# Kernel tuning notes

Hardware: AMD Instinct MI355X
Metric: run time of the kernel (lower is better)

Reference implementation:

```python
import jax, jax.numpy as jnp
import numpy as np

N = 50000
E = 800000
EP = 200000
IN_C = 128
HID = 128


def setup_inputs() -> dict:
    key = jax.random.key(0)
    ks = jax.random.split(key, 10)
    x = jax.random.normal(ks[0], (N, IN_C), dtype=jnp.float32)
    edge_index = jax.random.randint(ks[1], (2, E), 0, N, dtype=jnp.int64)
    pred_edges = jax.random.randint(ks[2], (2, EP), 0, N, dtype=jnp.int64)
    s_in = 1.0 / np.sqrt(IN_C)
    s_h = 1.0 / np.sqrt(HID)
    W1l = jax.random.normal(ks[3], (IN_C, HID), dtype=jnp.float32) * s_in
    W1r = jax.random.normal(ks[4], (IN_C, HID), dtype=jnp.float32) * s_in
    b1 = jnp.zeros((HID,), dtype=jnp.float32)
    W2l = jax.random.normal(ks[5], (HID, HID), dtype=jnp.float32) * s_h
    W2r = jax.random.normal(ks[6], (HID, HID), dtype=jnp.float32) * s_h
    b2 = jnp.zeros((HID,), dtype=jnp.float32)
    return {"x": x, "W1l": W1l, "b1": b1, "W1r": W1r,
            "W2l": W2l, "b2": b2, "W2r": W2r,
            "edge_index": edge_index, "pred_edges": pred_edges}


def _sage_conv(h, Wl, b, Wr, src, dst, n_nodes):
    # PyG SAGEConv (aggr='mean'): out = lin_l(mean_j x_j) + lin_r(x_i)
    msg = h[src]                                              # (E, D) gather
    agg = jax.ops.segment_sum(msg, dst, num_segments=n_nodes)  # (N, D) scatter-add
    deg = jax.ops.segment_sum(jnp.ones((src.shape[0],), h.dtype), dst,
                              num_segments=n_nodes)
    agg = agg / jnp.maximum(deg, 1.0)[:, None]                # mean (0 for isolated)
    return agg @ Wl + b + h @ Wr


def reference(x, W1l, b1, W1r, W2l, b2, W2r, edge_index, pred_edges):
    n_nodes = x.shape[0]
    src, dst = edge_index[0], edge_index[1]
    h = jax.nn.relu(_sage_conv(x, W1l, b1, W1r, src, dst, n_nodes))
    z = _sage_conv(h, W2l, b2, W2r, src, dst, n_nodes)
    ps, pd = pred_edges[0], pred_edges[1]
    return jnp.sum(z[ps] * z[pd], axis=-1)  # (E_pred,) logits
```

## Files before the change

### kernel.cpp

```cpp
#include <hip/hip_runtime.h>

#define D 128

typedef __attribute__((ext_vector_type(8))) short short8;
typedef __attribute__((ext_vector_type(4))) float f32x4;

__device__ inline unsigned int f2bf_bits(float f) {
    unsigned int u = __float_as_uint(f);
    return (u + 0x7FFFu + ((u >> 16) & 1u)) >> 16;
}

__global__ __launch_bounds__(256) void cast_bf16_kernel(const float* __restrict__ in,
                                                        unsigned short* __restrict__ outb,
                                                        int n4,
                                                        int* __restrict__ chist,
                                                        int* __restrict__ csrpad) {
    if (blockIdx.x == gridDim.x - 1) {
        int t = threadIdx.x;
        chist[t] = 0;
        if (t < 16) csrpad[t] = 0;
        return;
    }
    int i = blockIdx.x * blockDim.x + threadIdx.x;
    if (i >= n4) return;
    f32x4 v = *(const f32x4*)(in + (size_t)i * 4);
    ushort4 o;
    o.x = (unsigned short)f2bf_bits(v.x);
    o.y = (unsigned short)f2bf_bits(v.y);
    o.z = (unsigned short)f2bf_bits(v.z);
    o.w = (unsigned short)f2bf_bits(v.w);
    *(ushort4*)(outb + (size_t)i * 4) = o;
}

__global__ __launch_bounds__(256) void coarse_count_kernel(const int* __restrict__ dst,
                                                           int* __restrict__ chist, int E) {
    __shared__ int h[256];
    h[threadIdx.x] = 0;
    __syncthreads();
    const int stride = gridDim.x * 256;
    for (int e = blockIdx.x * 256 + threadIdx.x; e < E; e += stride)
        atomicAdd(&h[dst[e] >> 8], 1);
    __syncthreads();
    int v = h[threadIdx.x];
    if (v) atomicAdd(&chist[threadIdx.x], v);
}

__global__ __launch_bounds__(256) void scan256_kernel(const int* __restrict__ chist,
                                                      int* __restrict__ cbase,
                                                      int* __restrict__ gcur) {
    __shared__ int wsum[4];
    const int t = threadIdx.x, lane = t & 63, wv = t >> 6;
    int v = chist[t];
    int s = v;
#pragma unroll
    for (int o = 1; o < 64; o <<= 1) {
        int u = __shfl_up(s, o, 64);
        if (lane >= o) s += u;
    }
    if (lane == 63) wsum[wv] = s;
    __syncthreads();
    int add = 0;
    for (int w = 0; w < wv; ++w) add += wsum[w];
    cbase[t + 1] = s + add;
    if (t == 0) cbase[0] = 0;
    gcur[t] = s + add - v;
}

#define CCHUNK 4096
__global__ __launch_bounds__(256) void coarse_scatter_kernel(
    const int* __restrict__ src, const int* __restrict__ dst,
    int* __restrict__ gcur, unsigned int* __restrict__ centries, int E)
{
    __shared__ int h[256];
    __shared__ int base[256];
    __shared__ unsigned int stage[CCHUNK];
    const int t = threadIdx.x;
    const int e0 = blockIdx.x * CCHUNK;
    h[t] = 0;
    __syncthreads();
#pragma unroll
    for (int i = 0; i < 16; ++i) {
        int e = e0 + i * 256 + t;
        unsigned int u = 0xFFFFFFFFu;
        if (e < E) {
            int d = dst[e];
            int s = src[e];
            int b = d >> 8;
            u = ((unsigned)b << 24) | ((unsigned)s << 8) | (unsigned)(d & 255);
            atomicAdd(&h[b], 1);
        }
        stage[i * 256 + t] = u;
    }
    __syncthreads();
    base[t] = atomicAdd(&gcur[t], h[t]);
    __syncthreads();
    h[t] = 0;
    __syncthreads();
#pragma unroll
    for (int i = 0; i < 16; ++i) {
        unsigned int u = stage[i * 256 + t];
        if (u != 0xFFFFFFFFu) {
            int b = u >> 24;
            int r = atomicAdd(&h[b], 1);
            centries[base[b] + r] = u & 0x00FFFFFFu;
        }
    }
}

#define DCAP 8192
__global__ __launch_bounds__(256) void fine_bucket_kernel(
    const unsigned int* __restrict__ centries,
    const int* __restrict__ cbase,
    int* __restrict__ offo, int* __restrict__ csr, int N, int E)
{
    __shared__ int h[256], ex[256], wsum[4];
    __shared__ int stg[DCAP];
    const int t = threadIdx.x, lane = t & 63, wv = t >> 6;
    const int b = blockIdx.x;
    const int s0 = cbase[b];
    const int cnt = cbase[b + 1] - s0;
    h[t] = 0;
    __syncthreads();
    for (int i = t; i < cnt; i += 256)
        atomicAdd(&h[centries[s0 + i] & 255], 1);
    __syncthreads();
    int v = h[t], s = v;
#pragma unroll
    for (int o = 1; o < 64; o <<= 1) {
        int u = __shfl_up(s, o, 64);
        if (lane >= o) s += u;
    }
    if (lane == 63) wsum[wv] = s;
    __syncthreads();
    int add = 0;
    for (int w = 0; w < wv; ++w) add += wsum[w];
    const int exc = s + add - v;
    ex[t] = exc;
    const int dg = b * 256 + t;
    if (dg < N) offo[dg] = s0 + exc;
    if (b == 0 && t == 0) offo[N] = E;
    h[t] = 0;
    __syncthreads();
    if (cnt <= DCAP) {
        for (int i = t; i < cnt; i += 256) {
            unsigned int u = centries[s0 + i];
            int dl = u & 255;
            int r = atomicAdd(&h[dl], 1);
            stg[ex[dl] + r] = (int)(u >> 8);
        }
        __syncthreads();
        for (int i = t; i < cnt; i += 256)
            csr[s0 + i] = stg[i];
    } else {
        for (int i = t; i < cnt; i += 256) {
            unsigned int u = centries[s0 + i];
            int dl = u & 255;
            int r = atomicAdd(&h[dl], 1);
            csr[s0 + ex[dl] + r] = (int)(u >> 8);
        }
    }
}

__global__ __launch_bounds__(256) void wsplit_kernel(const float* __restrict__ W1l,
                                                     const float* __restrict__ W1r,
                                                     const float* __restrict__ W2l,
                                                     const float* __restrict__ W2r,
                                                     unsigned short* __restrict__ h1,
                                                     unsigned short* __restrict__ l1,
                                                     unsigned short* __restrict__ h2,
                                                     unsigned short* __restrict__ l2) {
    int gidx = blockIdx.x * 256 + threadIdx.x;
    int sel = gidx >> 15;
    int idx = gidx & 32767;
    int t = idx >> 12;
    int ks = (idx >> 9) & 7;
    int lane = (idx >> 3) & 63;
    int j = idx & 7;
    int q = lane >> 4, r16 = lane & 15;
    int k = ks * 32 + q * 8 + j;
    int c = t * 16 + r16;
    const float* Wl = sel ? W2l : W1l;
    const float* Wr = sel ? W2r : W1r;
    float v = (k < 128) ? Wl[k * 128 + c] : Wr[(k - 128) * 128 + c];
    unsigned int h = f2bf_bits(v);
    float hf = __uint_as_float(h << 16);
    unsigned int l = f2bf_bits(v - hf);
    (sel ? h2 : h1)[idx] = (unsigned short)h;
    (sel ? l2 : l1)[idx] = (unsigned short)l;
}

__global__ __launch_bounds__(256) void gather_mean_kernel(
    const unsigned short* __restrict__ featbf,
    const int* __restrict__ off,
    const int* __restrict__ csr,
    float* __restrict__ aggp,
    int n_nodes)
{
    const int hw = (blockIdx.x * 256 + threadIdx.x) >> 5;
    const int l5 = threadIdx.x & 31;
    if (hw >= n_nodes) return;
    const unsigned short* fb = featbf + (size_t)l5 * 4;
    const int start = off[hw];
    const int end = off[hw + 1];
    f32x4 acc = {0.f, 0.f, 0.f, 0.f};
    for (int e = start; e < end; e += 16) {
        int4 ia = *(const int4*)(csr + e);
        int4 ib = *(const int4*)(csr + e + 4);
        int4 ic = *(const int4*)(csr + e + 8);
        int4 id = *(const int4*)(csr + e + 12);
        uint2 r[16];
        r[0]  = *(const uint2*)(fb + (size_t)ia.x * D);
        r[1]  = *(const uint2*)(fb + (size_t)ia.y * D);
        r[2]  = *(const uint2*)(fb + (size_t)ia.z * D);
        r[3]  = *(const uint2*)(fb + (size_t)ia.w * D);
        r[4]  = *(const uint2*)(fb + (size_t)ib.x * D);
        r[5]  = *(const uint2*)(fb + (size_t)ib.y * D);
        r[6]  = *(const uint2*)(fb + (size_t)ib.z * D);
        r[7]  = *(const uint2*)(fb + (size_t)ib.w * D);
        r[8]  = *(const uint2*)(fb + (size_t)ic.x * D);
        r[9]  = *(const uint2*)(fb + (size_t)ic.y * D);
        r[10] = *(const uint2*)(fb + (size_t)ic.z * D);
        r[11] = *(const uint2*)(fb + (size_t)ic.w * D);
        r[12] = *(const uint2*)(fb + (size_t)id.x * D);
        r[13] = *(const uint2*)(fb + (size_t)id.y * D);
        r[14] = *(const uint2*)(fb + (size_t)id.z * D);
        r[15] = *(const uint2*)(fb + (size_t)id.w * D);
#pragma unroll
        for (int p = 0; p < 16; ++p) {
            uint2 rv = r[p];
            if (e + p >= end) { rv.x = 0u; rv.y = 0u; }
            acc.x += __uint_as_float(rv.x << 16);
            acc.y += __uint_as_float(rv.x & 0xffff0000u);
            acc.z += __uint_as_float(rv.y << 16);
            acc.w += __uint_as_float(rv.y & 0xffff0000u);
        }
    }
    float dinv = 1.0f / (float)max(end - start, 1);
    acc *= dinv;
    const int tile = hw >> 4, r16 = hw & 15;
    const int ks = l5 >> 3, q = (l5 & 7) >> 1, jb = (l5 & 1) * 4;
    const size_t p = ((size_t)(tile * 4 + ks) * 64 + q * 16 + r16) * 8 + jb;
    *(f32x4*)(aggp + p) = acc;
}

__global__ __launch_bounds__(256) void sage_gemm_kernel(
    const float* __restrict__ aggp,
    const float* __restrict__ selfm,
    const unsigned short* __restrict__ wpk_hi,
    const unsigned short* __restrict__ wpk_lo,
    const float* __restrict__ bias,
    float* __restrict__ outp,
    unsigned short* __restrict__ outbf,
    int ntiles, int self_packed, int do_relu)
{
    const int wv = threadIdx.x >> 6;
    const int lane = threadIdx.x & 63;
    const int tile = blockIdx.x * 4 + wv;
    if (tile >= ntiles) return;
    const int q = lane >> 4, r16 = lane & 15;
    const int n0w = tile * 16;

    f32x4 acc8[8];
#pragma unroll
    for (int t = 0; t < 8; ++t) acc8[t] = (f32x4){0.f, 0.f, 0.f, 0.f};

    const float* ap = aggp + (size_t)tile * 2048 + lane * 8;
    const float* spk = selfm + (size_t)tile * 2048 + lane * 8;
    const float* spr = selfm + (size_t)(n0w + r16) * D + q * 8;

    for (int ks = 0; ks < 8; ++ks) {
        f32x4 a0, a1;
        if (ks < 4) {
            a0 = *(const f32x4*)(ap + ks * 512);
            a1 = *(const f32x4*)(ap + ks * 512 + 4);
        } else if (self_packed) {
            a0 = *(const f32x4*)(spk + (ks - 4) * 512);
            a1 = *(const f32x4*)(spk + (ks - 4) * 512 + 4);
        } else {
            a0 = *(const f32x4*)(spr + (ks - 4) * 32);
            a1 = *(const f32x4*)(spr + (ks - 4) * 32 + 4);
        }
        short8 BH[8], BL[8];
        const unsigned short* bh = wpk_hi + (size_t)ks * 512 + lane * 8;
        const unsigned short* bl = wpk_lo + (size_t)ks * 512 + lane * 8;
#pragma unroll
        for (int t = 0; t < 8; ++t) {
            BH[t] = *(const short8*)(bh + (size_t)t * 4096);
            BL[t] = *(const short8*)(bl + (size_t)t * 4096);
        }
        short8 ahi, alo;
#pragma unroll
        for (int i = 0; i < 8; ++i) {
            float vv = (i < 4) ? a0[i] : a1[i - 4];
            unsigned int h = f2bf_bits(vv);
            float hf = __uint_as_float(h << 16);
            unsigned int l = f2bf_bits(vv - hf);
            ahi[i] = (short)h;
            alo[i] = (short)l;
        }
#pragma unroll
        for (int t = 0; t < 8; ++t) {
            acc8[t] = __builtin_amdgcn_mfma_f32_16x16x32_bf16(ahi, BH[t], acc8[t], 0, 0, 0);
            acc8[t] = __builtin_amdgcn_mfma_f32_16x16x32_bf16(alo, BH[t], acc8[t], 0, 0, 0);
            acc8[t] = __builtin_amdgcn_mfma_f32_16x16x32_bf16(ahi, BL[t], acc8[t], 0, 0, 0);
        }
    }

#pragma unroll
    for (int t = 0; t < 8; ++t) {
        const float bv = bias[t * 16 + r16];
#pragma unroll
        for (int r = 0; r < 4; ++r) {
            float vv = acc8[t][r] + bv;
            if (do_relu) vv = fmaxf(vv, 0.f);
            if (outp) {
                const size_t p = ((size_t)(tile * 4 + (t >> 1)) * 64
                                  + ((t & 1) * 2 + (r16 >> 3)) * 16 + q * 4 + r) * 8
                                 + (r16 & 7);
                outp[p] = vv;
            }
            if (outbf) {
                outbf[(size_t)(n0w + q * 4 + r) * D + t * 16 + r16] =
                    (unsigned short)f2bf_bits(vv);
            }
        }
    }
}

__global__ __launch_bounds__(256) void pred_kernel(const unsigned short* __restrict__ zbf,
                                                   const int* __restrict__ ps,
                                                   const int* __restrict__ pd,
                                                   float* __restrict__ out, int EP) {
    int idx = blockIdx.x * blockDim.x + threadIdx.x;
    int e = idx >> 5;
    if (e >= EP) return;
    int l = idx & 31;
    const unsigned short* fb = zbf + (size_t)l * 4;
    uint2 ra = *(const uint2*)(fb + (size_t)ps[e] * D);
    uint2 rb = *(const uint2*)(fb + (size_t)pd[e] * D);
    float p = __uint_as_float(ra.x << 16)         * __uint_as_float(rb.x << 16)
            + __uint_as_float(ra.x & 0xffff0000u) * __uint_as_float(rb.x & 0xffff0000u)
            + __uint_as_float(ra.y << 16)         * __uint_as_float(rb.y << 16)
            + __uint_as_float(ra.y & 0xffff0000u) * __uint_as_float(rb.y & 0xffff0000u);
#pragma unroll
    for (int off = 16; off > 0; off >>= 1) p += __shfl_xor(p, off, 32);
    if (l == 0) out[e] = p;
}

extern "C" void kernel_launch(void* const* d_in, const int* in_sizes, int n_in,
                              void* d_out, int out_size, void* d_ws, size_t ws_size,
                              hipStream_t stream) {
    const float* x   = (const float*)d_in[0];
    const float* W1l = (const float*)d_in[1];
    const float* b1  = (const float*)d_in[2];
    const float* W1r = (const float*)d_in[3];
    const float* W2l = (const float*)d_in[4];
    const float* b2  = (const float*)d_in[5];
    const float* W2r = (const float*)d_in[6];
    const int* edge_index = (const int*)d_in[7];
    const int* pred_edges = (const int*)d_in[8];
    float* out = (float*)d_out;

    const int N  = in_sizes[0] / D;
    const int E  = in_sizes[7] / 2;
    const int EP = in_sizes[8] / 2;

    const int* src = edge_index;
    const int* dst = edge_index + E;
    const int* ps  = pred_edges;
    const int* pd  = pred_edges + EP;

    int* chist   = (int*)d_ws;
    int* cbase   = chist + 256;
    int* gcur    = cbase + 272;
    int* off     = gcur + 256;
    unsigned int* centries = (unsigned int*)(off + 50016);
    int* csr     = (int*)(centries + E);
    float* aggp  = (float*)(csr + E + 16);
    float* hpk   = aggp + (size_t)N * D;
    unsigned short* w1_hi = (unsigned short*)(hpk + (size_t)N * D);
    unsigned short* w1_lo = w1_hi + 32768;
    unsigned short* w2_hi = w1_lo + 32768;
    unsigned short* w2_lo = w2_hi + 32768;
    unsigned short* fbf   = w2_lo + 32768;

    const int nblk_gather = (N * 32 + 255) / 256;
    const int ntiles = N / 16;
    const int nblk_gemm = (ntiles + 3) / 4;
    const int ncast = (N * D / 4 + 255) / 256;
    const int nbC = (E + CCHUNK - 1) / CCHUNK;
    const int nbD = (N + 255) / 256;

    wsplit_kernel<<<256, 256, 0, stream>>>(W1l, W1r, W2l, W2r, w1_hi, w1_lo, w2_hi, w2_lo);
    cast_bf16_kernel<<<ncast + 1, 256, 0, stream>>>(x, fbf, N * D / 4, chist, csr + E);

    coarse_count_kernel<<<256, 256, 0, stream>>>(dst, chist, E);
    scan256_kernel<<<1, 256, 0, stream>>>(chist, cbase, gcur);
    coarse_scatter_kernel<<<nbC, 256, 0, stream>>>(src, dst, gcur, centries, E);
    fine_bucket_kernel<<<nbD, 256, 0, stream>>>(centries, cbase, off, csr, N, E);

    gather_mean_kernel<<<nblk_gather, 256, 0, stream>>>(fbf, off, csr, aggp, N);
    sage_gemm_kernel<<<nblk_gemm, 256, 0, stream>>>(aggp, x, w1_hi, w1_lo, b1,
                                                    hpk, fbf, ntiles, 0, 1);
    gather_mean_kernel<<<nblk_gather, 256, 0, stream>>>(fbf, off, csr, aggp, N);
    sage_gemm_kernel<<<nblk_gemm, 256, 0, stream>>>(aggp, hpk, w2_hi, w2_lo, b2,
                                                    (float*)nullptr, fbf, ntiles, 1, 0);
    pred_kernel<<<(EP * 32 + 255) / 256, 256, 0, stream>>>(fbf, ps, pd, out, EP);
}
```

Before: 257.3 us.

## Store activations as bf16 hi/lo pairs and widen gather loads to 16 bytes

```diff
diff --git a/kernel.cpp b/kernel.cpp
--- a/kernel.cpp
+++ b/kernel.cpp
@@ -10,26 +10,61 @@
     return (u + 0x7FFFu + ((u >> 16) & 1u)) >> 16;
 }
 
-__global__ __launch_bounds__(256) void cast_bf16_kernel(const float* __restrict__ in,
-                                                        unsigned short* __restrict__ outb,
-                                                        int n4,
-                                                        int* __restrict__ chist,
-                                                        int* __restrict__ csrpad) {
-    if (blockIdx.x == gridDim.x - 1) {
-        int t = threadIdx.x;
+__device__ inline float bfhi(unsigned int u) { return __uint_as_float(u << 16); }
+__device__ inline float bflo(unsigned int u) { return __uint_as_float(u & 0xffff0000u); }
+
+__global__ __launch_bounds__(256) void prep_kernel(
+    const float* __restrict__ x,
+    const float* __restrict__ W1l, const float* __restrict__ W1r,
+    const float* __restrict__ W2l, const float* __restrict__ W2r,
+    unsigned short* __restrict__ xbf, unsigned short* __restrict__ xlo,
+    unsigned short* __restrict__ h1, unsigned short* __restrict__ l1,
+    unsigned short* __restrict__ h2, unsigned short* __restrict__ l2,
+    int n4, int ncast, int* __restrict__ chist, int* __restrict__ csrpad)
+{
+    const int b = blockIdx.x;
+    const int t = threadIdx.x;
+    if (b < ncast) {
+        int i = b * 256 + t;
+        if (i >= n4) return;
+        f32x4 v = *(const f32x4*)(x + (size_t)i * 4);
+        ushort4 oh, ol;
+        {
+            unsigned int h; float hf;
+            h = f2bf_bits(v.x); hf = __uint_as_float(h << 16);
+            oh.x = (unsigned short)h; ol.x = (unsigned short)f2bf_bits(v.x - hf);
+            h = f2bf_bits(v.y); hf = __uint_as_float(h << 16);
+            oh.y = (unsigned short)h; ol.y = (unsigned short)f2bf_bits(v.y - hf);
+            h = f2bf_bits(v.z); hf = __uint_as_float(h << 16);
+            oh.z = (unsigned short)h; ol.z = (unsigned short)f2bf_bits(v.z - hf);
+            h = f2bf_bits(v.w); hf = __uint_as_float(h << 16);
+            oh.w = (unsigned short)h; ol.w = (unsigned short)f2bf_bits(v.w - hf);
+        }
+        *(ushort4*)(xbf + (size_t)i * 4) = oh;
+        *(ushort4*)(xlo + (size_t)i * 4) = ol;
+    } else if (b < ncast + 256) {
+        int gidx = (b - ncast) * 256 + t;
+        int sel = gidx >> 15;
+        int idx = gidx & 32767;
+        int tt = idx >> 12;
+        int ks = (idx >> 9) & 7;
+        int lane = (idx >> 3) & 63;
+        int j = idx & 7;
+        int qq = lane >> 4, r16 = lane & 15;
+        int k = ks * 32 + qq * 8 + j;
+        int c = tt * 16 + r16;
+        const float* Wl = sel ? W2l : W1l;
+        const float* Wr = sel ? W2r : W1r;
+        float v = (k < 128) ? Wl[k * 128 + c] : Wr[(k - 128) * 128 + c];
+        unsigned int h = f2bf_bits(v);
+        float hf = __uint_as_float(h << 16);
+        unsigned int l = f2bf_bits(v - hf);
+        (sel ? h2 : h1)[idx] = (unsigned short)h;
+        (sel ? l2 : l1)[idx] = (unsigned short)l;
+    } else {
         chist[t] = 0;
         if (t < 16) csrpad[t] = 0;
-        return;
-    }
-    int i = blockIdx.x * blockDim.x + threadIdx.x;
-    if (i >= n4) return;
-    f32x4 v = *(const f32x4*)(in + (size_t)i * 4);
-    ushort4 o;
-    o.x = (unsigned short)f2bf_bits(v.x);
-    o.y = (unsigned short)f2bf_bits(v.y);
-    o.z = (unsigned short)f2bf_bits(v.z);
-    o.w = (unsigned short)f2bf_bits(v.w);
-    *(ushort4*)(outb + (size_t)i * 4) = o;
+    }
 }
 
 __global__ __launch_bounds__(256) void coarse_count_kernel(const int* __restrict__ dst,
@@ -161,97 +196,81 @@
     }
 }
 
-__global__ __launch_bounds__(256) void wsplit_kernel(const float* __restrict__ W1l,
-                                                     const float* __restrict__ W1r,
-                                                     const float* __restrict__ W2l,
-                                                     const float* __restrict__ W2r,
-                                                     unsigned short* __restrict__ h1,
-                                                     unsigned short* __restrict__ l1,
-                                                     unsigned short* __restrict__ h2,
-                                                     unsigned short* __restrict__ l2) {
-    int gidx = blockIdx.x * 256 + threadIdx.x;
-    int sel = gidx >> 15;
-    int idx = gidx & 32767;
-    int t = idx >> 12;
-    int ks = (idx >> 9) & 7;
-    int lane = (idx >> 3) & 63;
-    int j = idx & 7;
-    int q = lane >> 4, r16 = lane & 15;
-    int k = ks * 32 + q * 8 + j;
-    int c = t * 16 + r16;
-    const float* Wl = sel ? W2l : W1l;
-    const float* Wr = sel ? W2r : W1r;
-    float v = (k < 128) ? Wl[k * 128 + c] : Wr[(k - 128) * 128 + c];
-    unsigned int h = f2bf_bits(v);
-    float hf = __uint_as_float(h << 16);
-    unsigned int l = f2bf_bits(v - hf);
-    (sel ? h2 : h1)[idx] = (unsigned short)h;
-    (sel ? l2 : l1)[idx] = (unsigned short)l;
-}
-
 __global__ __launch_bounds__(256) void gather_mean_kernel(
     const unsigned short* __restrict__ featbf,
     const int* __restrict__ off,
     const int* __restrict__ csr,
-    float* __restrict__ aggp,
+    unsigned short* __restrict__ agg_hi,
+    unsigned short* __restrict__ agg_lo,
     int n_nodes)
 {
-    const int hw = (blockIdx.x * 256 + threadIdx.x) >> 5;
-    const int l5 = threadIdx.x & 31;
+    const int hw = (blockIdx.x * 256 + threadIdx.x) >> 4;
+    const int L = threadIdx.x & 15;
     if (hw >= n_nodes) return;
-    const unsigned short* fb = featbf + (size_t)l5 * 4;
+    const unsigned short* fb = featbf + (size_t)L * 8;
     const int start = off[hw];
     const int end = off[hw + 1];
-    f32x4 acc = {0.f, 0.f, 0.f, 0.f};
+    float acc[8] = {0.f, 0.f, 0.f, 0.f, 0.f, 0.f, 0.f, 0.f};
     for (int e = start; e < end; e += 16) {
         int4 ia = *(const int4*)(csr + e);
         int4 ib = *(const int4*)(csr + e + 4);
         int4 ic = *(const int4*)(csr + e + 8);
         int4 id = *(const int4*)(csr + e + 12);
-        uint2 r[16];
-        r[0]  = *(const uint2*)(fb + (size_t)ia.x * D);
-        r[1]  = *(const uint2*)(fb + (size_t)ia.y * D);
-        r[2]  = *(const uint2*)(fb + (size_t)ia.z * D);
-        r[3]  = *(const uint2*)(fb + (size_t)ia.w * D);
-        r[4]  = *(const uint2*)(fb + (size_t)ib.x * D);
-        r[5]  = *(const uint2*)(fb + (size_t)ib.y * D);
-        r[6]  = *(const uint2*)(fb + (size_t)ib.z * D);
-        r[7]  = *(const uint2*)(fb + (size_t)ib.w * D);
-        r[8]  = *(const uint2*)(fb + (size_t)ic.x * D);
-        r[9]  = *(const uint2*)(fb + (size_t)ic.y * D);
-        r[10] = *(const uint2*)(fb + (size_t)ic.z * D);
-        r[11] = *(const uint2*)(fb + (size_t)ic.w * D);
-        r[12] = *(const uint2*)(fb + (size_t)id.x * D);
-        r[13] = *(const uint2*)(fb + (size_t)id.y * D);
-        r[14] = *(const uint2*)(fb + (size_t)id.z * D);
-        r[15] = *(const uint2*)(fb + (size_t)id.w * D);
+        uint4 r[16];
+        r[0]  = *(const uint4*)(fb + (size_t)ia.x * D);
+        r[1]  = *(const uint4*)(fb + (size_t)ia.y * D);
+        r[2]  = *(const uint4*)(fb + (size_t)ia.z * D);
+        r[3]  = *(const uint4*)(fb + (size_t)ia.w * D);
+        r[4]  = *(const uint4*)(fb + (size_t)ib.x * D);
+        r[5]  = *(const uint4*)(fb + (size_t)ib.y * D);
+        r[6]  = *(const uint4*)(fb + (size_t)ib.z * D);
+        r[7]  = *(const uint4*)(fb + (size_t)ib.w * D);
+        r[8]  = *(const uint4*)(fb + (size_t)ic.x * D);
+        r[9]  = *(const uint4*)(fb + (size_t)ic.y * D);
+        r[10] = *(const uint4*)(fb + (size_t)ic.z * D);
+        r[11] = *(const uint4*)(fb + (size_t)ic.w * D);
+        r[12] = *(const uint4*)(fb + (size_t)id.x * D);
+        r[13] = *(const uint4*)(fb + (size_t)id.y * D);
+        r[14] = *(const uint4*)(fb + (size_t)id.z * D);
+        r[15] = *(const uint4*)(fb + (size_t)id.w * D);
 #pragma unroll
         for (int p = 0; p < 16; ++p) {
-            uint2 rv = r[p];
-            if (e + p >= end) { rv.x = 0u; rv.y = 0u; }
-            acc.x += __uint_as_float(rv.x << 16);
-            acc.y += __uint_as_float(rv.x & 0xffff0000u);
-            acc.z += __uint_as_float(rv.y << 16);
-            acc.w += __uint_as_float(rv.y & 0xffff0000u);
-        }
-    }
-    float dinv = 1.0f / (float)max(end - start, 1);
-    acc *= dinv;
+            uint4 rv = r[p];
+            if (e + p >= end) { rv.x = 0u; rv.y = 0u; rv.z = 0u; rv.w = 0u; }
+            acc[0] += bfhi(rv.x); acc[1] += bflo(rv.x);
+            acc[2] += bfhi(rv.y); acc[3] += bflo(rv.y);
+            acc[4] += bfhi(rv.z); acc[5] += bflo(rv.z);
+            acc[6] += bfhi(rv.w); acc[7] += bflo(rv.w);
+        }
+    }
+    const float dinv = 1.0f / (float)max(end - start, 1);
+    short8 hi8, lo8;
+#pragma unroll
+    for (int i = 0; i < 8; ++i) {
+        float v = acc[i] * dinv;
+        unsigned int h = f2bf_bits(v);
+        float hf = __uint_as_float(h << 16);
+        hi8[i] = (short)h;
+        lo8[i] = (short)f2bf_bits(v - hf);
+    }
     const int tile = hw >> 4, r16 = hw & 15;
-    const int ks = l5 >> 3, q = (l5 & 7) >> 1, jb = (l5 & 1) * 4;
-    const size_t p = ((size_t)(tile * 4 + ks) * 64 + q * 16 + r16) * 8 + jb;
-    *(f32x4*)(aggp + p) = acc;
+    const int ks = L >> 2, qq = L & 3;
+    const size_t p = ((size_t)(tile * 4 + ks) * 64 + qq * 16 + r16) * 8;
+    *(short8*)(agg_hi + p) = hi8;
+    *(short8*)(agg_lo + p) = lo8;
 }
 
 __global__ __launch_bounds__(256) void sage_gemm_kernel(
-    const float* __restrict__ aggp,
-    const float* __restrict__ selfm,
+    const unsigned short* __restrict__ agg_hi,
+    const unsigned short* __restrict__ agg_lo,
+    const unsigned short* __restrict__ self_hi,
+    const unsigned short* __restrict__ self_lo,
     const unsigned short* __restrict__ wpk_hi,
     const unsigned short* __restrict__ wpk_lo,
     const float* __restrict__ bias,
-    float* __restrict__ outp,
-    unsigned short* __restrict__ outbf,
-    int ntiles, int self_packed, int do_relu)
+    unsigned short* __restrict__ out_hi,
+    unsigned short* __restrict__ out_lo,
+    int ntiles, int do_relu)
 {
     const int wv = threadIdx.x >> 6;
     const int lane = threadIdx.x & 63;
@@ -264,21 +283,19 @@
 #pragma unroll
     for (int t = 0; t < 8; ++t) acc8[t] = (f32x4){0.f, 0.f, 0.f, 0.f};
 
-    const float* ap = aggp + (size_t)tile * 2048 + lane * 8;
-    const float* spk = selfm + (size_t)tile * 2048 + lane * 8;
-    const float* spr = selfm + (size_t)(n0w + r16) * D + q * 8;
+    const unsigned short* aph = agg_hi + (size_t)tile * 2048 + lane * 8;
+    const unsigned short* apl = agg_lo + (size_t)tile * 2048 + lane * 8;
+    const unsigned short* sph = self_hi + (size_t)(n0w + r16) * D + q * 8;
+    const unsigned short* spl = self_lo + (size_t)(n0w + r16) * D + q * 8;
 
     for (int ks = 0; ks < 8; ++ks) {
-        f32x4 a0, a1;
+        short8 ahi, alo;
         if (ks < 4) {
-            a0 = *(const f32x4*)(ap + ks * 512);
-            a1 = *(const f32x4*)(ap + ks * 512 + 4);
-        } else if (self_packed) {
-            a0 = *(const f32x4*)(spk + (ks - 4) * 512);
-            a1 = *(const f32x4*)(spk + (ks - 4) * 512 + 4);
+            ahi = *(const short8*)(aph + ks * 512);
+            alo = *(const short8*)(apl + ks * 512);
         } else {
-            a0 = *(const f32x4*)(spr + (ks - 4) * 32);
-            a1 = *(const f32x4*)(spr + (ks - 4) * 32 + 4);
+            ahi = *(const short8*)(sph + (ks - 4) * 32);
+            alo = *(const short8*)(spl + (ks - 4) * 32);
         }
         short8 BH[8], BL[8];
         const unsigned short* bh = wpk_hi + (size_t)ks * 512 + lane * 8;
@@ -287,16 +304,6 @@
         for (int t = 0; t < 8; ++t) {
             BH[t] = *(const short8*)(bh + (size_t)t * 4096);
             BL[t] = *(const short8*)(bl + (size_t)t * 4096);
-        }
-        short8 ahi, alo;
-#pragma unroll
-        for (int i = 0; i < 8; ++i) {
-            float vv = (i < 4) ? a0[i] : a1[i - 4];
-            unsigned int h = f2bf_bits(vv);
-            float hf = __uint_as_float(h << 16);
-            unsigned int l = f2bf_bits(vv - hf);
-            ahi[i] = (short)h;
-            alo[i] = (short)l;
         }
 #pragma unroll
         for (int t = 0; t < 8; ++t) {
@@ -313,15 +320,12 @@
         for (int r = 0; r < 4; ++r) {
             float vv = acc8[t][r] + bv;
             if (do_relu) vv = fmaxf(vv, 0.f);
-            if (outp) {
-                const size_t p = ((size_t)(tile * 4 + (t >> 1)) * 64
-                                  + ((t & 1) * 2 + (r16 >> 3)) * 16 + q * 4 + r) * 8
-                                 + (r16 & 7);
-                outp[p] = vv;
-            }
-            if (outbf) {
-                outbf[(size_t)(n0w + q * 4 + r) * D + t * 16 + r16] =
-                    (unsigned short)f2bf_bits(vv);
+            const size_t o = (size_t)(n0w + q * 4 + r) * D + t * 16 + r16;
+            unsigned int h = f2bf_bits(vv);
+            out_hi[o] = (unsigned short)h;
+            if (out_lo) {
+                float hf = __uint_as_float(h << 16);
+                out_lo[o] = (unsigned short)f2bf_bits(vv - hf);
             }
         }
     }
@@ -331,20 +335,20 @@
                                                    const int* __restrict__ ps,
                                                    const int* __restrict__ pd,
                                                    float* __restrict__ out, int EP) {
-    int idx = blockIdx.x * blockDim.x + threadIdx.x;
-    int e = idx >> 5;
+    int idx = blockIdx.x * 256 + threadIdx.x;
+    int e = idx >> 4;
     if (e >= EP) return;
-    int l = idx & 31;
-    const unsigned short* fb = zbf + (size_t)l * 4;
-    uint2 ra = *(const uint2*)(fb + (size_t)ps[e] * D);
-    uint2 rb = *(const uint2*)(fb + (size_t)pd[e] * D);
-    float p = __uint_as_float(ra.x << 16)         * __uint_as_float(rb.x << 16)
-            + __uint_as_float(ra.x & 0xffff0000u) * __uint_as_float(rb.x & 0xffff0000u)
-            + __uint_as_float(ra.y << 16)         * __uint_as_float(rb.y << 16)
-            + __uint_as_float(ra.y & 0xffff0000u) * __uint_as_float(rb.y & 0xffff0000u);
-#pragma unroll
-    for (int off = 16; off > 0; off >>= 1) p += __shfl_xor(p, off, 32);
-    if (l == 0) out[e] = p;
+    int L = idx & 15;
+    const unsigned short* fb = zbf + (size_t)L * 8;
+    uint4 ra = *(const uint4*)(fb + (size_t)ps[e] * D);
+    uint4 rb = *(const uint4*)(fb + (size_t)pd[e] * D);
+    float p = bfhi(ra.x) * bfhi(rb.x) + bflo(ra.x) * bflo(rb.x)
+            + bfhi(ra.y) * bfhi(rb.y) + bflo(ra.y) * bflo(rb.y)
+            + bfhi(ra.z) * bfhi(rb.z) + bflo(ra.z) * bflo(rb.z)
+            + bfhi(ra.w) * bfhi(rb.w) + bflo(ra.w) * bflo(rb.w);
+#pragma unroll
+    for (int off = 8; off > 0; off >>= 1) p += __shfl_xor(p, off, 16);
+    if (L == 0) out[e] = p;
 }
 
 extern "C" void kernel_launch(void* const* d_in, const int* in_sizes, int n_in,
@@ -376,34 +380,42 @@
     int* off     = gcur + 256;
     unsigned int* centries = (unsigned int*)(off + 50016);
     int* csr     = (int*)(centries + E);
-    float* aggp  = (float*)(csr + E + 16);
-    float* hpk   = aggp + (size_t)N * D;
-    unsigned short* w1_hi = (unsigned short*)(hpk + (size_t)N * D);
+    unsigned short* w1_hi = (unsigned short*)(csr + E + 16);
     unsigned short* w1_lo = w1_hi + 32768;
     unsigned short* w2_hi = w1_lo + 32768;
     unsigned short* w2_lo = w2_hi + 32768;
-    unsigned short* fbf   = w2_lo + 32768;
-
-    const int nblk_gather = (N * 32 + 255) / 256;
+    unsigned short* xbf   = w2_lo + 32768;
+    unsigned short* xlo   = xbf + (size_t)N * D;
+    unsigned short* hbf   = xlo + (size_t)N * D;
+    unsigned short* hlo   = hbf + (size_t)N * D;
+    unsigned short* zbf   = hlo + (size_t)N * D;
+    unsigned short* agg_hi = zbf + (size_t)N * D;
+    unsigned short* agg_lo = agg_hi + (size_t)N * D;
+
+    const int n4 = N * D / 4;
+    const int ncast = (n4 + 255) / 256;
+    const int nblk_gather = (N * 16 + 255) / 256;
     const int ntiles = N / 16;
     const int nblk_gemm = (ntiles + 3) / 4;
-    const int ncast = (N * D / 4 + 255) / 256;
     const int nbC = (E + CCHUNK - 1) / CCHUNK;
     const int nbD = (N + 255) / 256;
-
-    wsplit_kernel<<<256, 256, 0, stream>>>(W1l, W1r, W2l, W2r, w1_hi, w1_lo, w2_hi, w2_lo);
-    cast_bf16_kernel<<<ncast + 1, 256, 0, stream>>>(x, fbf, N * D / 4, chist, csr + E);
+    const int nblk_pred = (EP * 16 + 255) / 256;
+
+    prep_kernel<<<ncast + 257, 256, 0, stream>>>(x, W1l, W1r, W2l, W2r,
+                                                 xbf, xlo, w1_hi, w1_lo, w2_hi, w2_lo,
+                                                 n4, ncast, chist, csr + E);
 
     coarse_count_kernel<<<256, 256, 0, stream>>>(dst, chist, E);
     scan256_kernel<<<1, 256, 0, stream>>>(chist, cbase, gcur);
     coarse_scatter_kernel<<<nbC, 256, 0, stream>>>(src, dst, gcur, centries, E);
     fine_bucket_kernel<<<nbD, 256, 0, stream>>>(centries, cbase, off, csr, N, E);
 
-    gather_mean_kernel<<<nblk_gather, 256, 0, stream>>>(fbf, off, csr, aggp, N);
-    sage_gemm_kernel<<<nblk_gemm, 256, 0, stream>>>(aggp, x, w1_hi, w1_lo, b1,
-                                                    hpk, fbf, ntiles, 0, 1);
-    gather_mean_kernel<<<nblk_gather, 256, 0, stream>>>(fbf, off, csr, aggp, N);
-    sage_gemm_kernel<<<nblk_gemm, 256, 0, stream>>>(aggp, hpk, w2_hi, w2_lo, b2,
-                                                    (float*)nullptr, fbf, ntiles, 1, 0);
-    pred_kernel<<<(EP * 32 + 255) / 256, 256, 0, stream>>>(fbf, ps, pd, out, EP);
-}
+    gather_mean_kernel<<<nblk_gather, 256, 0, stream>>>(xbf, off, csr, agg_hi, agg_lo, N);
+    sage_gemm_kernel<<<nblk_gemm, 256, 0, stream>>>(agg_hi, agg_lo, xbf, xlo,
+                                                    w1_hi, w1_lo, b1, hbf, hlo, ntiles, 1);
+    gather_mean_kernel<<<nblk_gather, 256, 0, stream>>>(hbf, off, csr, agg_hi, agg_lo, N);
+    sage_gemm_kernel<<<nblk_gemm, 256, 0, stream>>>(agg_hi, agg_lo, hbf, hlo,
+                                                    w2_hi, w2_lo, b2, zbf, (unsigned short*)nullptr,
+                                                    ntiles, 0);
+    pred_kernel<<<nblk_pred, 256, 0, stream>>>(zbf, ps, pd, out, EP);
+}
```

Result: slower. 310.7 us (+20.8%).
